# Performance work log

Hardware: AMD Instinct MI355X
Metric: run time of the kernel (lower is better)

## Reference

```python
import jax, jax.numpy as jnp
import numpy as np

B, T, N, M, P = 1024, 128, 128, 256, 256


def _lstm_step(x, h, c, Wih, Whh, bih, bhh):
    # PyTorch LSTM cell: gates ordered i, f, g, o
    g = x @ Wih.T + bih + h @ Whh.T + bhh
    i, f, gg, o = jnp.split(g, 4, axis=-1)
    c_new = jax.nn.sigmoid(f) * c + jax.nn.sigmoid(i) * jnp.tanh(gg)
    h_new = jax.nn.sigmoid(o) * jnp.tanh(c_new)
    return h_new, c_new


def darnn_forward(enc_data, dec_data, enc_Wih, enc_Whh, enc_bih, enc_bhh,
                  We, Ue, ve, Wd, Ud, vd, wt_w, wt_b,
                  dec_Wih, dec_Whh, dec_bih, dec_bhh, l1_w, l1_b, l2_w, l2_b):
    Bsz, Tlen, n = enc_data.shape
    m = enc_Whh.shape[1]
    p = dec_Whh.shape[1]
    # ---- Encoder with input attention ----
    # U_e(data.permute(0,2,1)): (B, n, T); constant across time steps
    Ue_data = jnp.einsum('btn,st->bns', enc_data, Ue)
    def enc_step(carry, x_t):
        h, c = carry                                   # (B, m) each
        q = jnp.concatenate([h, c], axis=-1)           # (B, 2m)
        wq = q @ We.T                                  # (B, T)
        score = jnp.tanh(wq[:, None, :] + Ue_data) @ ve  # (B, n)
        alpha = jax.nn.softmax(score, axis=-1)
        h, c = _lstm_step(alpha * x_t, h, c, enc_Wih, enc_Whh, enc_bih, enc_bhh)
        return (h, c), h
    h0 = jnp.zeros((Bsz, m), enc_data.dtype)
    (_, _), Hs = jax.lax.scan(enc_step, (h0, h0), jnp.swapaxes(enc_data, 0, 1))
    H = jnp.swapaxes(Hs, 0, 1)                         # (B, T, m)
    # ---- Decoder with temporal attention ----
    UH = jnp.einsum('btm,um->btu', H, Ud)              # (B, T, m); constant
    def attn_ctx(d, s):
        q = jnp.concatenate([d, s], axis=-1)           # (B, 2p)
        wq = q @ Wd.T                                  # (B, m)
        score = jnp.tanh(wq[:, None, :] + UH) @ vd     # (B, T)
        beta = jax.nn.softmax(score, axis=-1)
        return jnp.einsum('bt,btm->bm', beta, H)       # (B, m)
    def dec_step(carry, y):
        d, s = carry
        ctx = attn_ctx(d, s)
        y_tilde = jnp.concatenate([y, ctx], axis=-1) @ wt_w.T + wt_b  # (B, 1)
        d, s = _lstm_step(y_tilde, d, s, dec_Wih, dec_Whh, dec_bih, dec_bhh)
        return (d, s), None
    d0 = jnp.zeros((Bsz, p), enc_data.dtype)
    ys = jnp.swapaxes(dec_data[:, :Tlen - 1, :], 0, 1)  # (T-1, B, 1)
    (d, s), _ = jax.lax.scan(dec_step, (d0, d0), ys)
    ctx = attn_ctx(d, s)
    out = jnp.concatenate([d, ctx], axis=-1)            # (B, p + m)
    out = jax.nn.relu(out @ l1_w.T + l1_b) @ l2_w.T + l2_b
    return out.reshape(-1)


def setup_inputs() -> dict:
    key = jax.random.key(0)
    ks = jax.random.split(key, 22)
    f = lambda k, shape: jax.random.normal(k, shape, jnp.float32) * 0.05
    return {
        'enc_data': jax.random.normal(ks[0], (B, T, N), jnp.float32),
        'dec_data': jax.random.normal(ks[1], (B, T, 1), jnp.float32),
        'enc_Wih': f(ks[2], (4 * M, N)), 'enc_Whh': f(ks[3], (4 * M, M)),
        'enc_bih': f(ks[4], (4 * M,)), 'enc_bhh': f(ks[5], (4 * M,)),
        'We': f(ks[6], (T, 2 * M)), 'Ue': f(ks[7], (T, T)), 've': f(ks[8], (T,)),
        'Wd': f(ks[9], (M, 2 * P)), 'Ud': f(ks[10], (M, M)), 'vd': f(ks[11], (M,)),
        'wt_w': f(ks[12], (1, M + 1)), 'wt_b': f(ks[13], (1,)),
        'dec_Wih': f(ks[14], (4 * P, 1)), 'dec_Whh': f(ks[15], (4 * P, P)),
        'dec_bih': f(ks[16], (4 * P,)), 'dec_bhh': f(ks[17], (4 * P,)),
        'l1_w': f(ks[18], (P, M + P)), 'l1_b': f(ks[19], (P,)),
        'l2_w': f(ks[20], (1, P)), 'l2_b': f(ks[21], (1,)),
    }


def reference(enc_data, dec_data, enc_Wih, enc_Whh, enc_bih, enc_bhh,
              We, Ue, ve, Wd, Ud, vd, wt_w, wt_b,
              dec_Wih, dec_Whh, dec_bih, dec_bhh, l1_w, l1_b, l2_w, l2_b):
    return darnn_forward(enc_data, dec_data, enc_Wih, enc_Whh, enc_bih, enc_bhh,
                         We, Ue, ve, Wd, Ud, vd, wt_w, wt_b,
                         dec_Wih, dec_Whh, dec_bih, dec_bhh, l1_w, l1_b, l2_w, l2_b)
```

## Files before the change

kernel.cpp:

```cpp
#include <hip/hip_runtime.h>

typedef unsigned short ushort_t;
typedef unsigned char u8_t;
typedef unsigned int u32_t;
typedef float f32x2 __attribute__((ext_vector_type(2)));

static constexpr int BATCH = 1024;
static constexpr int TT = 128;
static constexpr int NN = 128;
static constexpr int MM = 256;

__device__ __forceinline__ float bf2f(ushort_t u) {
    union { unsigned int i; float f; } v;
    v.i = ((unsigned int)u) << 16;
    return v.f;
}
__device__ __forceinline__ ushort_t f2bf(float f) {
    union { unsigned int i; float f; } v;
    v.f = f;
    unsigned int i = v.i;
    return (ushort_t)((i + 0x7FFFu + ((i >> 16) & 1u)) >> 16);
}
__device__ __forceinline__ u32_t pk2bf(float lo, float hi) {
    return (u32_t)f2bf(lo) | ((u32_t)f2bf(hi) << 16);
}
__device__ __forceinline__ float dot2bf(u32_t a, u32_t b, float c) {
    float d;
    asm("v_dot2_f32_bf16 %0, %1, %2, %3" : "=v"(d) : "v"(a), "v"(b), "v"(c));
    return d;
}
__device__ __forceinline__ u32_t permb(u32_t s0, u32_t s1, u32_t sel) {
    u32_t d;
    asm("v_perm_b32 %0, %1, %2, %3" : "=v"(d) : "v"(s0), "v"(s1), "v"(sel));
    return d;
}
__device__ __forceinline__ void unp8(const int4 w, float* o) {
    union { unsigned int i; float f; } v;
    v.i = ((unsigned int)w.x) << 16;        o[0] = v.f;
    v.i = ((unsigned int)w.x) & 0xffff0000u; o[1] = v.f;
    v.i = ((unsigned int)w.y) << 16;        o[2] = v.f;
    v.i = ((unsigned int)w.y) & 0xffff0000u; o[3] = v.f;
    v.i = ((unsigned int)w.z) << 16;        o[4] = v.f;
    v.i = ((unsigned int)w.z) & 0xffff0000u; o[5] = v.f;
    v.i = ((unsigned int)w.w) << 16;        o[6] = v.f;
    v.i = ((unsigned int)w.w) & 0xffff0000u; o[7] = v.f;
}
__device__ __forceinline__ void unp4(const int2 w, float* o) {
    union { unsigned int i; float f; } v;
    v.i = ((unsigned int)w.x) << 16;        o[0] = v.f;
    v.i = ((unsigned int)w.x) & 0xffff0000u; o[1] = v.f;
    v.i = ((unsigned int)w.y) << 16;        o[2] = v.f;
    v.i = ((unsigned int)w.y) & 0xffff0000u; o[3] = v.f;
}
__device__ __forceinline__ void unp8f8(const int2 w, float* o) {
    f32x2 a = __builtin_amdgcn_cvt_pk_f32_fp8(w.x, false);
    f32x2 b = __builtin_amdgcn_cvt_pk_f32_fp8(w.x, true);
    f32x2 c = __builtin_amdgcn_cvt_pk_f32_fp8(w.y, false);
    f32x2 d = __builtin_amdgcn_cvt_pk_f32_fp8(w.y, true);
    o[0] = a.x; o[1] = a.y; o[2] = b.x; o[3] = b.y;
    o[4] = c.x; o[5] = c.y; o[6] = d.x; o[7] = d.y;
}
__device__ __forceinline__ float tanh_fast(float x) {
    float e = __expf(2.0f * x);
    return 1.0f - __fdividef(2.0f, e + 1.0f);
}
__device__ __forceinline__ float sig_fast(float x) {
    return __fdividef(1.0f, 1.0f + __expf(-x));
}

template<bool WBF16, bool TRANSW, int CMODE, bool RELU>
__global__ __launch_bounds__(256) void gemm_k(
    const float* __restrict__ A1, int lda1, long sA1z, int K1,
    const float* __restrict__ A2, int lda2, int K2,
    const void* __restrict__ W1v, int ldw1, long sW1z,
    const void* __restrict__ W2v, int ldw2,
    const float* __restrict__ bias1,
    void* __restrict__ Cv, int ldc, long sCz)
{
    __shared__ float As[32][68];
    __shared__ float Ws[32][68];
    const int tid = threadIdx.x;
    const int z = blockIdx.z;
    const int m0 = blockIdx.y * 64;
    const int g0 = blockIdx.x * 64;
    const int tm = tid & 15, tn = tid >> 4;
    float acc[4][4];
#pragma unroll
    for (int i = 0; i < 4; ++i)
#pragma unroll
        for (int j = 0; j < 4; ++j) acc[i][j] = 0.0f;

    for (int phase = 0; phase < 2; ++phase) {
        const float* A = (phase == 0) ? (A1 + (long)z * sA1z) : A2;
        const int lda = (phase == 0) ? lda1 : lda2;
        const int K = (phase == 0) ? K1 : K2;
        const int ldw = (phase == 0) ? ldw1 : ldw2;
        const void* Wv = (phase == 0) ? W1v : W2v;
        const long woff = (phase == 0) ? (long)z * sW1z : 0;
        if (A == nullptr || Wv == nullptr || K <= 0) continue;

        for (int k0 = 0; k0 < K; k0 += 32) {
            const int rem = K - k0;
            {
                const int tr0 = tid >> 3;
                const int tk = (tid & 7) * 4;
#pragma unroll
                for (int pass = 0; pass < 2; ++pass) {
                    const int m = tr0 + pass * 32;
                    const float* p = A + (long)(m0 + m) * lda + k0 + tk;
#pragma unroll
                    for (int j = 0; j < 4; ++j) {
                        float v = 0.0f;
                        if (tk + j < rem) v = p[j];
                        As[tk + j][m] = v;
                    }
                }
            }
            if constexpr (TRANSW) {
                const float* W = (const float*)Wv + woff;
                const int gq = (tid & 15) * 4;
                const int kr = tid >> 4;
#pragma unroll
                for (int pass = 0; pass < 2; ++pass) {
                    const int k = kr + pass * 16;
                    const float* p = W + (long)(k0 + k) * ldw + g0 + gq;
                    const bool ok = (k < rem);
#pragma unroll
                    for (int j = 0; j < 4; ++j) {
                        float v = 0.0f;
                        if (ok) v = p[j];
                        Ws[k][gq + j] = v;
                    }
                }
            } else if constexpr (WBF16) {
                const ushort_t* W = (const ushort_t*)Wv + woff;
                const int g = tid >> 2;
                const int tk = (tid & 3) * 8;
                const ushort_t* p = W + (long)(g0 + g) * ldw + k0 + tk;
#pragma unroll
                for (int j = 0; j < 8; ++j) {
                    float v = 0.0f;
                    if (tk + j < rem) v = bf2f(p[j]);
                    Ws[tk + j][g] = v;
                }
            } else {
                const float* W = (const float*)Wv + woff;
                const int tr0 = tid >> 3;
                const int tk = (tid & 7) * 4;
#pragma unroll
                for (int pass = 0; pass < 2; ++pass) {
                    const int g = tr0 + pass * 32;
                    const float* p = W + (long)(g0 + g) * ldw + k0 + tk;
#pragma unroll
                    for (int j = 0; j < 4; ++j) {
                        float v = 0.0f;
                        if (tk + j < rem) v = p[j];
                        Ws[tk + j][g] = v;
                    }
                }
            }
            __syncthreads();
#pragma unroll
            for (int kk = 0; kk < 32; ++kk) {
                const float4 av = *(const float4*)&As[kk][tm * 4];
                const float4 bv = *(const float4*)&Ws[kk][tn * 4];
                const float a[4] = {av.x, av.y, av.z, av.w};
                const float b[4] = {bv.x, bv.y, bv.z, bv.w};
#pragma unroll
                for (int i = 0; i < 4; ++i)
#pragma unroll
                    for (int j = 0; j < 4; ++j)
                        acc[i][j] = fmaf(a[i], b[j], acc[i][j]);
            }
            __syncthreads();
        }
    }
#pragma unroll
    for (int i = 0; i < 4; ++i) {
        const long m = m0 + tm * 4 + i;
        if constexpr (CMODE == 2) {
            float v[4];
#pragma unroll
            for (int j = 0; j < 4; ++j) {
                v[j] = acc[i][j];
                if (bias1) v[j] += bias1[g0 + tn * 4 + j];
                if (RELU) v[j] = fmaxf(v[j], 0.0f);
            }
            int pk = __builtin_amdgcn_cvt_pk_fp8_f32(v[0], v[1], 0, false);
            pk = __builtin_amdgcn_cvt_pk_fp8_f32(v[2], v[3], pk, true);
            *(unsigned int*)((u8_t*)Cv + (long)z * sCz + m * ldc + g0 + tn * 4) =
                (unsigned int)pk;
        } else {
#pragma unroll
            for (int j = 0; j < 4; ++j) {
                const int g = g0 + tn * 4 + j;
                float v = acc[i][j];
                if (bias1) v += bias1[g];
                if (RELU) v = fmaxf(v, 0.0f);
                if constexpr (CMODE == 1)
                    ((ushort_t*)Cv)[(long)z * sCz + m * ldc + g] = f2bf(v);
                else
                    ((float*)Cv)[(long)z * sCz + m * ldc + g] = v;
            }
        }
    }
}

__global__ void prep_encw_k(const float* __restrict__ Wih, const float* __restrict__ Whh,
                            ushort_t* __restrict__ dst) {
    int i = blockIdx.x * 256 + threadIdx.x;
    if (i >= 384 * 1024) return;
    int k = i >> 10, col = i & 1023, u = col >> 2, q = col & 3, g = q * 256 + u;
    float v = (k < 128) ? Wih[g * 128 + k] : Whh[g * 256 + (k - 128)];
    dst[(k >> 1) * 2048 + u * 8 + q * 2 + (k & 1)] = f2bf(v);
}

__global__ void prep_decw_k(const float* __restrict__ Wih, const float* __restrict__ Whh,
                            ushort_t* __restrict__ dst) {
    int i = blockIdx.x * 256 + threadIdx.x;
    if (i >= 257 * 1024) return;
    int k = i >> 10, col = i & 1023, u = col >> 2, q = col & 3, g = q * 256 + u;
    float v = (k == 0) ? Wih[g] : Whh[g * 256 + (k - 1)];
    ushort_t b = f2bf(v);
    if (k == 0) {
        dst[col] = b;
    } else {
        int kk = k - 1;
        dst[1024 + (kk >> 1) * 2048 + u * 8 + q * 2 + (kk & 1)] = b;
    }
}

__global__ void transpose_k(const float* __restrict__ src, float* __restrict__ dst,
                            int R, int C) {
    int i = blockIdx.x * 256 + threadIdx.x;
    if (i < R * C) { int r = i / C, c = i - r * C; dst[c * R + r] = src[i]; }
}

__global__ void packT_k(const float* __restrict__ src, ushort_t* __restrict__ dst,
                        int R, int C) {
    int i = blockIdx.x * 256 + threadIdx.x;
    if (i >= R * C) return;
    int s = i / C, k = i - s * C;
    dst[(k >> 1) * (2 * R) + (s >> 2) * 8 + (s & 3) * 2 + (k & 1)] = f2bf(src[i]);
}

__global__ __launch_bounds__(512) void enc_persist(
    const float* __restrict__ enc_data,
    const u8_t* __restrict__ D,
    const ushort_t* __restrict__ WeB,
    const float* __restrict__ ve,
    const ushort_t* __restrict__ WencB,
    const float* __restrict__ bih, const float* __restrict__ bhh,
    ushort_t* __restrict__ Hbf)
{
    const int tid = threadIdx.x;
    const int b0 = blockIdx.x * 4;
    __shared__ __align__(16) float cs[256][4];
    __shared__ __align__(16) u32_t qpk[256][4];
    __shared__ __align__(16) u32_t xtp[64][4];
    __shared__ __align__(16) float wqp[16][128][4];
    __shared__ __align__(16) float wqs[128][4];
    __shared__ __align__(16) float scp[8][4][128];
    __shared__ float gp[4][4][256];
    __shared__ float ves[128];

    if (tid < 128) ves[tid] = ve[tid];
    if (tid < 256) {
        const float4 z = make_float4(0.f, 0.f, 0.f, 0.f);
        *(float4*)cs[tid] = z;
    }
    {
        uint4 z4 = {0u, 0u, 0u, 0u};
        for (int i = tid; i < 256; i += 512) *(uint4*)qpk[i] = z4;
    }
    const int u = tid & 255;
    const int ks = tid >> 8;
    const float b_i = bih[u] + bhh[u];
    const float b_f = bih[256 + u] + bhh[256 + u];
    const float b_g = bih[512 + u] + bhh[512 + u];
    const float b_o = bih[768 + u] + bhh[768 + u];
    __syncthreads();

    const int kgq = tid >> 5, sv = tid & 31;
    const ushort_t* wq_w = WeB + (long)(kgq * 16) * 256 + sv * 8;
    const int nv = tid & 15, srow = (tid >> 4) & 3, ssl = tid >> 6;
    const u8_t* Dp0 = D + (long)(b0 + srow) * 16384 + (ssl * 16) * 128 + nv * 8;
    const ushort_t* gw = WencB + u * 8;

    float SVe = 0.0f;
#pragma unroll
    for (int s = 0; s < 16; ++s) SVe += ves[ssl * 16 + s];

    for (int t = 0; t < 128; ++t) {
        {
            float a[4][4];
#pragma unroll
            for (int m = 0; m < 4; ++m)
#pragma unroll
                for (int r = 0; r < 4; ++r) a[m][r] = 0.0f;
#pragma unroll 4
            for (int k2 = 0; k2 < 16; ++k2) {
                const uint4 wv = *(const uint4*)(wq_w + k2 * 256);
                const uint4 qv = *(const uint4*)qpk[kgq * 16 + k2];
                const u32_t wa[4] = {wv.x, wv.y, wv.z, wv.w};
                const u32_t qa[4] = {qv.x, qv.y, qv.z, qv.w};
#pragma unroll
                for (int m = 0; m < 4; ++m)
#pragma unroll
                    for (int r = 0; r < 4; ++r)
                        a[m][r] = dot2bf(wa[m], qa[r], a[m][r]);
            }
#pragma unroll
            for (int m = 0; m < 4; ++m)
                *(float4*)wqp[kgq][sv * 4 + m] = make_float4(a[m][0], a[m][1], a[m][2], a[m][3]);
        }
        __syncthreads();
        if (tid < 128) {
            float4 s = *(const float4*)wqp[0][tid];
#pragma unroll
            for (int g = 1; g < 16; ++g) {
                const float4 p = *(const float4*)wqp[g][tid];
                s.x += p.x; s.y += p.y; s.z += p.z; s.w += p.w;
            }
            *(float4*)wqs[tid] = s;
        }
        __syncthreads();
        {
            float a[8];
#pragma unroll
            for (int j = 0; j < 8; ++j) a[j] = 0.0f;
#pragma unroll 4
            for (int s = 0; s < 16; ++s) {
                const int sg = ssl * 16 + s;
                const float w2 = wqs[sg][srow] * 2.0f;
                const float vv = ves[sg];
                const int2 wv2 = *(const int2*)(Dp0 + s * 128);
                float d[8];
                unp8f8(wv2, d);
#pragma unroll
                for (int j = 0; j < 8; j += 2) {
                    const float eA = __expf(fminf(fmaf(d[j],     2.0f, w2), 43.0f));
                    const float eB = __expf(fminf(fmaf(d[j + 1], 2.0f, w2), 43.0f));
                    const float pA = eA + 1.0f, pB = eB + 1.0f;
                    const float rr = __fdividef(1.0f, pA * pB);
                    a[j]     = fmaf(vv, pB * rr, a[j]);
                    a[j + 1] = fmaf(vv, pA * rr, a[j + 1]);
                }
            }
            *(float4*)&scp[ssl][srow][nv * 8] =
                make_float4(fmaf(-2.f, a[0], SVe), fmaf(-2.f, a[1], SVe),
                            fmaf(-2.f, a[2], SVe), fmaf(-2.f, a[3], SVe));
            *(float4*)&scp[ssl][srow][nv * 8 + 4] =
                make_float4(fmaf(-2.f, a[4], SVe), fmaf(-2.f, a[5], SVe),
                            fmaf(-2.f, a[6], SVe), fmaf(-2.f, a[7], SVe));
        }
        __syncthreads();
        if (tid < 256) {
            const int w = tid >> 6, lane = tid & 63;
            float s0 = 0.0f, s1 = 0.0f;
#pragma unroll
            for (int g = 0; g < 8; ++g) {
                s0 += scp[g][w][lane];
                s1 += scp[g][w][lane + 64];
            }
            float mx = fmaxf(s0, s1);
            for (int o = 32; o > 0; o >>= 1) mx = fmaxf(mx, __shfl_xor(mx, o, 64));
            const float e0 = __expf(s0 - mx), e1 = __expf(s1 - mx);
            float sm = e0 + e1;
            for (int o = 32; o > 0; o >>= 1) sm += __shfl_xor(sm, o, 64);
            const float inv = __fdividef(1.0f, sm);
            const float* xp = enc_data + ((long)(b0 + w) * 128 + t) * 128;
            const float v0 = e0 * inv * xp[lane];
            const float v1 = e1 * inv * xp[lane + 64];
            const float p0 = __shfl_xor(v0, 1, 64);
            const float p1 = __shfl_xor(v1, 1, 64);
            if ((lane & 1) == 0) {
                xtp[lane >> 1][w] = pk2bf(v0, p0);
                xtp[32 + (lane >> 1)][w] = pk2bf(v1, p1);
            }
        }
        __syncthreads();
        float acc[4][4];
#pragma unroll
        for (int q = 0; q < 4; ++q)
#pragma unroll
            for (int r = 0; r < 4; ++r) acc[q][r] = 0.0f;
        if (ks == 0) {
#pragma unroll 4
            for (int p = 0; p < 64; ++p) {
                const uint4 wv = *(const uint4*)(gw + (long)p * 2048);
                const uint4 xv = *(const uint4*)xtp[p];
                const u32_t wa[4] = {wv.x, wv.y, wv.z, wv.w};
                const u32_t xa[4] = {xv.x, xv.y, xv.z, xv.w};
#pragma unroll
                for (int q = 0; q < 4; ++q)
#pragma unroll
                    for (int r = 0; r < 4; ++r)
                        acc[q][r] = dot2bf(wa[q], xa[r], acc[q][r]);
            }
#pragma unroll 4
            for (int p = 64; p < 96; ++p) {
                const uint4 wv = *(const uint4*)(gw + (long)p * 2048);
                const uint4 xv = *(const uint4*)qpk[p - 64];
                const u32_t wa[4] = {wv.x, wv.y, wv.z, wv.w};
                const u32_t xa[4] = {xv.x, xv.y, xv.z, xv.w};
#pragma unroll
                for (int q = 0; q < 4; ++q)
#pragma unroll
                    for (int r = 0; r < 4; ++r)
                        acc[q][r] = dot2bf(wa[q], xa[r], acc[q][r]);
            }
        } else {
#pragma unroll 4
            for (int p = 96; p < 192; ++p) {
                const uint4 wv = *(const uint4*)(gw + (long)p * 2048);
                const uint4 xv = *(const uint4*)qpk[p - 64];
                const u32_t wa[4] = {wv.x, wv.y, wv.z, wv.w};
                const u32_t xa[4] = {xv.x, xv.y, xv.z, xv.w};
#pragma unroll
                for (int q = 0; q < 4; ++q)
#pragma unroll
                    for (int r = 0; r < 4; ++r)
                        acc[q][r] = dot2bf(wa[q], xa[r], acc[q][r]);
            }
#pragma unroll
            for (int q = 0; q < 4; ++q)
#pragma unroll
                for (int r = 0; r < 4; ++r) gp[q][r][u] = acc[q][r];
        }
        __syncthreads();
        if (ks == 0) {
#pragma unroll
            for (int r = 0; r < 4; ++r) {
                const float iv = sig_fast(acc[0][r] + gp[0][r][u] + b_i);
                const float fv = sig_fast(acc[1][r] + gp[1][r][u] + b_f);
                const float gv = tanh_fast(acc[2][r] + gp[2][r][u] + b_g);
                const float ov = sig_fast(acc[3][r] + gp[3][r][u] + b_o);
                const float cn = fv * cs[u][r] + iv * gv;
                const float hn = ov * tanh_fast(cn);
                cs[u][r] = cn;
                const float hp = __shfl_xor(hn, 1, 64);
                const float cp = __shfl_xor(cn, 1, 64);
                if ((u & 1) == 0) {
                    qpk[u >> 1][r] = pk2bf(hn, hp);
                    qpk[128 + (u >> 1)][r] = pk2bf(cn, cp);
                }
                Hbf[((long)(b0 + r) * 128 + t) * 256 + u] = f2bf(hn);
            }
        }
        __syncthreads();
    }
}

__global__ __launch_bounds__(512) void dec_persist(
    const float* __restrict__ dec_data,
    const u8_t* __restrict__ UH2,
    const ushort_t* __restrict__ Hb,
    const ushort_t* __restrict__ WdB,
    const float* __restrict__ vd,
    const ushort_t* __restrict__ WdecB,
    const float* __restrict__ bih, const float* __restrict__ bhh,
    const float* __restrict__ wt_w, const float* __restrict__ wt_b,
    const float* __restrict__ l1T,
    const float* __restrict__ l1_b,
    const float* __restrict__ l2_w, const float* __restrict__ l2_b,
    float* __restrict__ out)
{
    const int tid = threadIdx.x;
    const int b0 = blockIdx.x * 4;
    __shared__ __align__(16) float ds4[256][4];
    __shared__ __align__(16) float ss4[256][4];
    __shared__ __align__(16) u32_t qpk[256][4];
    __shared__ __align__(16) float wqp[8][256][4];
    __shared__ __align__(16) float wqs[256][4];
    __shared__ __align__(16) float scp[8][4][128];
    __shared__ __align__(16) u32_t betap[64][4];
    __shared__ __align__(16) float ctxp[4][4][256];
    __shared__ __align__(16) float ctx4[256][4];
    __shared__ float gp[4][4][256];
    __shared__ __align__(16) float o14[256][4];
    __shared__ float vds[256];
    __shared__ float wt1s[256];
    __shared__ float l2s[256];
    __shared__ __align__(16) float yts[4];

    const int u = tid & 255;
    const int ks = tid >> 8;
    if (tid < 256) {
        vds[tid] = vd[tid];
        wt1s[tid] = wt_w[1 + tid];
        l2s[tid] = l2_w[tid];
        const float4 z = make_float4(0.f, 0.f, 0.f, 0.f);
        *(float4*)ds4[tid] = z;
        *(float4*)ss4[tid] = z;
    }
    {
        uint4 z4 = {0u, 0u, 0u, 0u};
        for (int i = tid; i < 256; i += 512) *(uint4*)qpk[i] = z4;
    }
    const float b_i = bih[u] + bhh[u];
    const float b_f = bih[256 + u] + bhh[256 + u];
    const float b_g = bih[512 + u] + bhh[512 + u];
    const float b_o = bih[768 + u] + bhh[768 + u];
    __syncthreads();

    const int kgq = tid >> 6, mv = tid & 63;
    const ushort_t* wq_w = WdB + (long)(kgq * 32) * 512 + mv * 8;
    const int tv = tid & 15, srow = (tid >> 4) & 3, usl = tid >> 6;
    const u8_t* up0 = UH2 + ((long)(b0 + srow) * 256 + usl * 32) * 128 + tv * 8;
    const int mv8 = tid & 31, crow = (tid >> 5) & 3, ssl2 = tid >> 7;
    const ushort_t* hp0 = Hb + ((long)(b0 + crow) * 128 + ssl2 * 32) * 256 + mv8 * 8;
    const ushort_t* gwp = WdecB + 1024 + u * 8;

    float SVd = 0.0f;
#pragma unroll
    for (int s = 0; s < 32; ++s) SVd += vds[usl * 32 + s];

    for (int td = 0; td < 128; ++td) {
        float gacc[4][4];
        {
            float a[4][4];
#pragma unroll
            for (int m = 0; m < 4; ++m)
#pragma unroll
                for (int r = 0; r < 4; ++r) a[m][r] = 0.0f;
#pragma unroll 4
            for (int k2 = 0; k2 < 32; ++k2) {
                const uint4 wv = *(const uint4*)(wq_w + k2 * 512);
                const uint4 qv = *(const uint4*)qpk[kgq * 32 + k2];
                const u32_t wa[4] = {wv.x, wv.y, wv.z, wv.w};
                const u32_t qa[4] = {qv.x, qv.y, qv.z, qv.w};
#pragma unroll
                for (int m = 0; m < 4; ++m)
#pragma unroll
                    for (int r = 0; r < 4; ++r)
                        a[m][r] = dot2bf(wa[m], qa[r], a[m][r]);
            }
#pragma unroll
            for (int m = 0; m < 4; ++m)
                *(float4*)wqp[kgq][mv * 4 + m] = make_float4(a[m][0], a[m][1], a[m][2], a[m][3]);
        }
        {
#pragma unroll
            for (int q = 0; q < 4; ++q)
#pragma unroll
                for (int r = 0; r < 4; ++r) gacc[q][r] = 0.0f;
            const int pbeg = ks * 64, pend = pbeg + 64;
#pragma unroll 4
            for (int p = pbeg; p < pend; ++p) {
                const uint4 wv = *(const uint4*)(gwp + (long)p * 2048);
                const uint4 xv = *(const uint4*)qpk[p];
                const u32_t wa[4] = {wv.x, wv.y, wv.z, wv.w};
                const u32_t xa[4] = {xv.x, xv.y, xv.z, xv.w};
#pragma unroll
                for (int q = 0; q < 4; ++q)
#pragma unroll
                    for (int r = 0; r < 4; ++r)
                        gacc[q][r] = dot2bf(wa[q], xa[r], gacc[q][r]);
            }
            if (ks != 0) {
#pragma unroll
                for (int q = 0; q < 4; ++q)
#pragma unroll
                    for (int r = 0; r < 4; ++r) gp[q][r][u] = gacc[q][r];
            }
        }
        __syncthreads();
        if (tid < 256) {
            float4 s = *(const float4*)wqp[0][tid];
#pragma unroll
            for (int g = 1; g < 8; ++g) {
                const float4 p = *(const float4*)wqp[g][tid];
                s.x += p.x; s.y += p.y; s.z += p.z; s.w += p.w;
            }
            *(float4*)wqs[tid] = s;
        }
        __syncthreads();
        {
            float a[8];
#pragma unroll
            for (int j = 0; j < 8; ++j) a[j] = 0.0f;
#pragma unroll 4
            for (int uu = 0; uu < 32; ++uu) {
                const int ug = usl * 32 + uu;
                const float w2 = wqs[ug][srow] * 2.0f;
                const float vv = vds[ug];
                const int2 wv2 = *(const int2*)(up0 + uu * 128);
                float d[8];
                unp8f8(wv2, d);
#pragma unroll
                for (int j = 0; j < 8; j += 2) {
                    const float eA = __expf(fminf(fmaf(d[j],     2.0f, w2), 43.0f));
                    const float eB = __expf(fminf(fmaf(d[j + 1], 2.0f, w2), 43.0f));
                    const float pA = eA + 1.0f, pB = eB + 1.0f;
                    const float rr = __fdividef(1.0f, pA * pB);
                    a[j]     = fmaf(vv, pB * rr, a[j]);
                    a[j + 1] = fmaf(vv, pA * rr, a[j + 1]);
                }
            }
            *(float4*)&scp[usl][srow][tv * 8] =
                make_float4(fmaf(-2.f, a[0], SVd), fmaf(-2.f, a[1], SVd),
                            fmaf(-2.f, a[2], SVd), fmaf(-2.f, a[3], SVd));
            *(float4*)&scp[usl][srow][tv * 8 + 4] =
                make_float4(fmaf(-2.f, a[4], SVd), fmaf(-2.f, a[5], SVd),
                            fmaf(-2.f, a[6], SVd), fmaf(-2.f, a[7], SVd));
        }
        __syncthreads();
        if (tid < 256) {
            const int w = tid >> 6, lane = tid & 63;
            float s0 = 0.0f, s1 = 0.0f;
#pragma unroll
            for (int g = 0; g < 8; ++g) {
                s0 += scp[g][w][lane];
                s1 += scp[g][w][lane + 64];
            }
            float mx = fmaxf(s0, s1);
            for (int o = 32; o > 0; o >>= 1) mx = fmaxf(mx, __shfl_xor(mx, o, 64));
            const float e0 = __expf(s0 - mx), e1 = __expf(s1 - mx);
            float sm = e0 + e1;
            for (int o = 32; o > 0; o >>= 1) sm += __shfl_xor(sm, o, 64);
            const float inv = __fdividef(1.0f, sm);
            const float bv0 = e0 * inv;
            const float bv1 = e1 * inv;
            const float q0 = __shfl_xor(bv0, 1, 64);
            const float q1 = __shfl_xor(bv1, 1, 64);
            if ((lane & 1) == 0) {
                betap[lane >> 1][w] = pk2bf(bv0, q0);
                betap[32 + (lane >> 1)][w] = pk2bf(bv1, q1);
            }
        }
        __syncthreads();
        {
            float c[8];
#pragma unroll
            for (int j = 0; j < 8; ++j) c[j] = 0.0f;
#pragma unroll 4
            for (int sp = 0; sp < 16; ++sp) {
                const u32_t bt = betap[ssl2 * 16 + sp][crow];
                const uint4 A = *(const uint4*)(hp0 + (2 * sp) * 256);
                const uint4 B = *(const uint4*)(hp0 + (2 * sp + 1) * 256);
                const u32_t Aa[4] = {A.x, A.y, A.z, A.w};
                const u32_t Ba[4] = {B.x, B.y, B.z, B.w};
#pragma unroll
                for (int x = 0; x < 4; ++x) {
                    const u32_t lo = permb(Aa[x], Ba[x], 0x01000504u);
                    const u32_t hi = permb(Aa[x], Ba[x], 0x03020706u);
                    c[2 * x]     = dot2bf(bt, lo, c[2 * x]);
                    c[2 * x + 1] = dot2bf(bt, hi, c[2 * x + 1]);
                }
            }
            *(float4*)&ctxp[ssl2][crow][mv8 * 8]     = make_float4(c[0], c[1], c[2], c[3]);
            *(float4*)&ctxp[ssl2][crow][mv8 * 8 + 4] = make_float4(c[4], c[5], c[6], c[7]);
        }
        __syncthreads();
        if (tid < 256) {
            const int m = tid;
            float cr[4];
#pragma unroll
            for (int r = 0; r < 4; ++r)
                cr[r] = ctxp[0][r][m] + ctxp[1][r][m] + ctxp[2][r][m] + ctxp[3][r][m];
            *(float4*)ctx4[m] = make_float4(cr[0], cr[1], cr[2], cr[3]);
        }
        __syncthreads();
        if (td == 127) break;
        if (tid < 256) {
            const int w = tid >> 6, lane = tid & 63;
            float s = ctx4[lane][w] * wt1s[lane]
                    + ctx4[lane + 64][w] * wt1s[lane + 64]
                    + ctx4[lane + 128][w] * wt1s[lane + 128]
                    + ctx4[lane + 192][w] * wt1s[lane + 192];
            for (int o = 32; o > 0; o >>= 1) s += __shfl_xor(s, o, 64);
            if (lane == 0)
                yts[w] = s + wt_b[0] + wt_w[0] * dec_data[(long)(b0 + w) * 128 + td];
        }
        __syncthreads();
        if (ks == 0) {
            float wy[4];
            unp4(*(const int2*)(WdecB + u * 4), wy);
            const float4 y4 = *(const float4*)yts;
            const float ya[4] = {y4.x, y4.y, y4.z, y4.w};
#pragma unroll
            for (int r = 0; r < 4; ++r) {
                const float iv = sig_fast(gacc[0][r] + gp[0][r][u] + wy[0] * ya[r] + b_i);
                const float fv = sig_fast(gacc[1][r] + gp[1][r][u] + wy[1] * ya[r] + b_f);
                const float gv = tanh_fast(gacc[2][r] + gp[2][r][u] + wy[2] * ya[r] + b_g);
                const float ov = sig_fast(gacc[3][r] + gp[3][r][u] + wy[3] * ya[r] + b_o);
                const float sn = fv * ss4[u][r] + iv * gv;
                const float dn = ov * tanh_fast(sn);
                ss4[u][r] = sn;
                ds4[u][r] = dn;
                const float dp = __shfl_xor(dn, 1, 64);
                const float sp = __shfl_xor(sn, 1, 64);
                if ((u & 1) == 0) {
                    qpk[u >> 1][r] = pk2bf(dn, dp);
                    qpk[128 + (u >> 1)][r] = pk2bf(sn, sp);
                }
            }
        }
        __syncthreads();
    }
    {
        const float* src = l1T + ks * 256 * 256;
        float a0 = 0, a1 = 0, a2 = 0, a3 = 0;
#pragma unroll 4
        for (int k = 0; k < 256; ++k) {
            const float w = src[k * 256 + u];
            const float4 q = (ks == 0) ? *(const float4*)ds4[k]
                                       : *(const float4*)ctx4[k];
            a0 = fmaf(q.x, w, a0); a1 = fmaf(q.y, w, a1);
            a2 = fmaf(q.z, w, a2); a3 = fmaf(q.w, w, a3);
        }
        if (ks == 1) {
            gp[0][0][u] = a0; gp[0][1][u] = a1; gp[0][2][u] = a2; gp[0][3][u] = a3;
        } else {
            gp[1][0][u] = a0; gp[1][1][u] = a1; gp[1][2][u] = a2; gp[1][3][u] = a3;
        }
    }
    __syncthreads();
    if (tid < 256) {
        const float bb = l1_b[tid];
        *(float4*)o14[tid] = make_float4(
            fmaxf(gp[0][0][tid] + gp[1][0][tid] + bb, 0.f),
            fmaxf(gp[0][1][tid] + gp[1][1][tid] + bb, 0.f),
            fmaxf(gp[0][2][tid] + gp[1][2][tid] + bb, 0.f),
            fmaxf(gp[0][3][tid] + gp[1][3][tid] + bb, 0.f));
    }
    __syncthreads();
    if (tid < 256) {
        const int w = tid >> 6, lane = tid & 63;
        float s = o14[lane][w] * l2s[lane]
                + o14[lane + 64][w] * l2s[lane + 64]
                + o14[lane + 128][w] * l2s[lane + 128]
                + o14[lane + 192][w] * l2s[lane + 192];
        for (int o = 32; o > 0; o >>= 1) s += __shfl_xor(s, o, 64);
        if (lane == 0) out[b0 + w] = s + l2_b[0];
    }
}

extern "C" void kernel_launch(void* const* d_in, const int* in_sizes, int n_in,
                              void* d_out, int out_size, void* d_ws, size_t ws_size,
                              hipStream_t stream)
{
    const float* enc_data = (const float*)d_in[0];
    const float* dec_data = (const float*)d_in[1];
    const float* enc_Wih  = (const float*)d_in[2];
    const float* enc_Whh  = (const float*)d_in[3];
    const float* enc_bih  = (const float*)d_in[4];
    const float* enc_bhh  = (const float*)d_in[5];
    const float* We   = (const float*)d_in[6];
    const float* Ue   = (const float*)d_in[7];
    const float* ve   = (const float*)d_in[8];
    const float* Wd   = (const float*)d_in[9];
    const float* Ud   = (const float*)d_in[10];
    const float* vd   = (const float*)d_in[11];
    const float* wt_w = (const float*)d_in[12];
    const float* wt_b = (const float*)d_in[13];
    const float* dec_Wih = (const float*)d_in[14];
    const float* dec_Whh = (const float*)d_in[15];
    const float* dec_bih = (const float*)d_in[16];
    const float* dec_bhh = (const float*)d_in[17];
    const float* l1_w = (const float*)d_in[18];
    const float* l1_b = (const float*)d_in[19];
    const float* l2_w = (const float*)d_in[20];
    const float* l2_b = (const float*)d_in[21];

    ushort_t* Hbf  = (ushort_t*)d_ws;
    u8_t* Dbf      = (u8_t*)(Hbf + (long)BATCH * TT * MM);
    u8_t* UHbf     = Dbf + (long)BATCH * TT * NN;
    ushort_t* WencB = (ushort_t*)(UHbf + (long)BATCH * MM * TT);
    ushort_t* WdecB = WencB + 384 * 1024;
    ushort_t* WeB   = WdecB + 257 * 1024;
    ushort_t* WdB   = WeB + 512 * 128;
    float* l1T      = (float*)(WdB + 512 * 256);

    prep_encw_k<<<1536, 256, 0, stream>>>(enc_Wih, enc_Whh, WencB);
    prep_decw_k<<<1028, 256, 0, stream>>>(dec_Wih, dec_Whh, WdecB);
    packT_k<<<(128 * 512 + 255) / 256, 256, 0, stream>>>(We, WeB, 128, 512);
    packT_k<<<(256 * 512 + 255) / 256, 256, 0, stream>>>(Wd, WdB, 256, 512);
    transpose_k<<<(256 * 512 + 255) / 256, 256, 0, stream>>>(l1_w, l1T, 256, 512);

    gemm_k<false, true, 2, false><<<dim3(NN / 64, TT / 64, BATCH), 256, 0, stream>>>(
        Ue, TT, 0, TT,
        nullptr, 0, 0,
        enc_data, NN, (long)TT * NN,
        nullptr, 0,
        nullptr,
        Dbf, NN, (long)TT * NN);

    enc_persist<<<256, 512, 0, stream>>>(enc_data, Dbf, WeB, ve, WencB,
                                         enc_bih, enc_bhh, Hbf);

    gemm_k<true, false, 2, false><<<dim3(TT / 64, MM / 64, BATCH), 256, 0, stream>>>(
        Ud, MM, 0, MM,
        nullptr, 0, 0,
        Hbf, MM, (long)TT * MM,
        nullptr, 0,
        nullptr,
        UHbf, TT, (long)MM * TT);

    dec_persist<<<256, 512, 0, stream>>>(dec_data, UHbf, Hbf, WdB, vd, WdecB,
                                         dec_bih, dec_bhh, wt_w, wt_b,
                                         l1T, l1_b, l2_w, l2_b, (float*)d_out);
}
```

Before: 8.004 ms.

## Prescale attention operands by 2·log2e and rebalance encoder gate GEMM across halves

Folds the 2·log2(e) factor of tanh into the packed We/Wd weights and the fp8 Ue·X and Ud·H projections, so the attention inner loop calls the raw v_exp_f32 on a plain add instead of a scaled __expf. In the encoder, the recurrent h/c part of the gate matvec is moved before the first barrier and split evenly across both thread halves, and the input part is also split in two. This overlaps work with the attention phase and balances the gate dot products, which were previously lopsided between ks halves. The fp8 storage now holds scaled values, which changes rounding and saturation range, and the clamp becomes 60.

```diff
diff --git a/kernel.cpp b/kernel.cpp
--- a/kernel.cpp
+++ b/kernel.cpp
@@ -9,6 +9,7 @@
 static constexpr int TT = 128;
 static constexpr int NN = 128;
 static constexpr int MM = 256;
+static constexpr float SC2LOG2E = 2.885390082f;
 
 __device__ __forceinline__ float bf2f(ushort_t u) {
     union { unsigned int i; float f; } v;
@@ -33,6 +34,11 @@
     u32_t d;
     asm("v_perm_b32 %0, %1, %2, %3" : "=v"(d) : "v"(s0), "v"(s1), "v"(sel));
     return d;
+}
+__device__ __forceinline__ float exp2_fast(float x) {
+    float r;
+    asm("v_exp_f32 %0, %1" : "=v"(r) : "v"(x));
+    return r;
 }
 __device__ __forceinline__ void unp8(const int4 w, float* o) {
     union { unsigned int i; float f; } v;
@@ -74,7 +80,7 @@
     const float* __restrict__ A2, int lda2, int K2,
     const void* __restrict__ W1v, int ldw1, long sW1z,
     const void* __restrict__ W2v, int ldw2,
-    const float* __restrict__ bias1,
+    const float* __restrict__ bias1, float oscale,
     void* __restrict__ Cv, int ldc, long sCz)
 {
     __shared__ float As[32][68];
@@ -182,7 +188,7 @@
             float v[4];
 #pragma unroll
             for (int j = 0; j < 4; ++j) {
-                v[j] = acc[i][j];
+                v[j] = acc[i][j] * oscale;
                 if (bias1) v[j] += bias1[g0 + tn * 4 + j];
                 if (RELU) v[j] = fmaxf(v[j], 0.0f);
             }
@@ -237,11 +243,11 @@
 }
 
 __global__ void packT_k(const float* __restrict__ src, ushort_t* __restrict__ dst,
-                        int R, int C) {
+                        int R, int C, float scale) {
     int i = blockIdx.x * 256 + threadIdx.x;
     if (i >= R * C) return;
     int s = i / C, k = i - s * C;
-    dst[(k >> 1) * (2 * R) + (s >> 2) * 8 + (s & 3) * 2 + (k & 1)] = f2bf(src[i]);
+    dst[(k >> 1) * (2 * R) + (s >> 2) * 8 + (s & 3) * 2 + (k & 1)] = f2bf(src[i] * scale);
 }
 
 __global__ __launch_bounds__(512) void enc_persist(
@@ -292,6 +298,11 @@
     for (int s = 0; s < 16; ++s) SVe += ves[ssl * 16 + s];
 
     for (int t = 0; t < 128; ++t) {
+        float gacc[4][4];
+#pragma unroll
+        for (int q = 0; q < 4; ++q)
+#pragma unroll
+            for (int r = 0; r < 4; ++r) gacc[q][r] = 0.0f;
         {
             float a[4][4];
 #pragma unroll
@@ -314,6 +325,21 @@
             for (int m = 0; m < 4; ++m)
                 *(float4*)wqp[kgq][sv * 4 + m] = make_float4(a[m][0], a[m][1], a[m][2], a[m][3]);
         }
+        {
+            const int pbeg = 64 + ks * 64, pend = pbeg + 64;
+#pragma unroll 4
+            for (int p = pbeg; p < pend; ++p) {
+                const uint4 wv = *(const uint4*)(gw + (long)p * 2048);
+                const uint4 xv = *(const uint4*)qpk[p - 64];
+                const u32_t wa[4] = {wv.x, wv.y, wv.z, wv.w};
+                const u32_t xa[4] = {xv.x, xv.y, xv.z, xv.w};
+#pragma unroll
+                for (int q = 0; q < 4; ++q)
+#pragma unroll
+                    for (int r = 0; r < 4; ++r)
+                        gacc[q][r] = dot2bf(wa[q], xa[r], gacc[q][r]);
+            }
+        }
         __syncthreads();
         if (tid < 128) {
             float4 s = *(const float4*)wqp[0][tid];
@@ -332,15 +358,15 @@
 #pragma unroll 4
             for (int s = 0; s < 16; ++s) {
                 const int sg = ssl * 16 + s;
-                const float w2 = wqs[sg][srow] * 2.0f;
+                const float w2 = wqs[sg][srow];
                 const float vv = ves[sg];
                 const int2 wv2 = *(const int2*)(Dp0 + s * 128);
                 float d[8];
                 unp8f8(wv2, d);
 #pragma unroll
                 for (int j = 0; j < 8; j += 2) {
-                    const float eA = __expf(fminf(fmaf(d[j],     2.0f, w2), 43.0f));
-                    const float eB = __expf(fminf(fmaf(d[j + 1], 2.0f, w2), 43.0f));
+                    const float eA = exp2_fast(fminf(d[j]     + w2, 60.0f));
+                    const float eB = exp2_fast(fminf(d[j + 1] + w2, 60.0f));
                     const float pA = eA + 1.0f, pB = eB + 1.0f;
                     const float rr = __fdividef(1.0f, pA * pB);
                     a[j]     = fmaf(vv, pB * rr, a[j]);
@@ -380,14 +406,10 @@
             }
         }
         __syncthreads();
-        float acc[4][4];
-#pragma unroll
-        for (int q = 0; q < 4; ++q)
-#pragma unroll
-            for (int r = 0; r < 4; ++r) acc[q][r] = 0.0f;
-        if (ks == 0) {
+        {
+            const int pbeg = ks * 32, pend = pbeg + 32;
 #pragma unroll 4
-            for (int p = 0; p < 64; ++p) {
+            for (int p = pbeg; p < pend; ++p) {
                 const uint4 wv = *(const uint4*)(gw + (long)p * 2048);
                 const uint4 xv = *(const uint4*)xtp[p];
                 const u32_t wa[4] = {wv.x, wv.y, wv.z, wv.w};
@@ -396,46 +418,23 @@
                 for (int q = 0; q < 4; ++q)
 #pragma unroll
                     for (int r = 0; r < 4; ++r)
-                        acc[q][r] = dot2bf(wa[q], xa[r], acc[q][r]);
-            }
-#pragma unroll 4
-            for (int p = 64; p < 96; ++p) {
-                const uint4 wv = *(const uint4*)(gw + (long)p * 2048);
-                const uint4 xv = *(const uint4*)qpk[p - 64];
-                const u32_t wa[4] = {wv.x, wv.y, wv.z, wv.w};
-                const u32_t xa[4] = {xv.x, xv.y, xv.z, xv.w};
+                        gacc[q][r] = dot2bf(wa[q], xa[r], gacc[q][r]);
+            }
+            if (ks != 0) {
 #pragma unroll
                 for (int q = 0; q < 4; ++q)
 #pragma unroll
-                    for (int r = 0; r < 4; ++r)
-                        acc[q][r] = dot2bf(wa[q], xa[r], acc[q][r]);
-            }
-        } else {
-#pragma unroll 4
-            for (int p = 96; p < 192; ++p) {
-                const uint4 wv = *(const uint4*)(gw + (long)p * 2048);
-                const uint4 xv = *(const uint4*)qpk[p - 64];
-                const u32_t wa[4] = {wv.x, wv.y, wv.z, wv.w};
-                const u32_t xa[4] = {xv.x, xv.y, xv.z, xv.w};
-#pragma unroll
-                for (int q = 0; q < 4; ++q)
-#pragma unroll
-                    for (int r = 0; r < 4; ++r)
-                        acc[q][r] = dot2bf(wa[q], xa[r], acc[q][r]);
-            }
-#pragma unroll
-            for (int q = 0; q < 4; ++q)
-#pragma unroll
-                for (int r = 0; r < 4; ++r) gp[q][r][u] = acc[q][r];
+                    for (int r = 0; r < 4; ++r) gp[q][r][u] = gacc[q][r];
+            }
         }
         __syncthreads();
         if (ks == 0) {
 #pragma unroll
             for (int r = 0; r < 4; ++r) {
-                const float iv = sig_fast(acc[0][r] + gp[0][r][u] + b_i);
-                const float fv = sig_fast(acc[1][r] + gp[1][r][u] + b_f);
-                const float gv = tanh_fast(acc[2][r] + gp[2][r][u] + b_g);
-                const float ov = sig_fast(acc[3][r] + gp[3][r][u] + b_o);
+                const float iv = sig_fast(gacc[0][r] + gp[0][r][u] + b_i);
+                const float fv = sig_fast(gacc[1][r] + gp[1][r][u] + b_f);
+                const float gv = tanh_fast(gacc[2][r] + gp[2][r][u] + b_g);
+                const float ov = sig_fast(gacc[3][r] + gp[3][r][u] + b_o);
                 const float cn = fv * cs[u][r] + iv * gv;
                 const float hn = ov * tanh_fast(cn);
                 cs[u][r] = cn;
@@ -583,15 +582,15 @@
 #pragma unroll 4
             for (int uu = 0; uu < 32; ++uu) {
                 const int ug = usl * 32 + uu;
-                const float w2 = wqs[ug][srow] * 2.0f;
+                const float w2 = wqs[ug][srow];
                 const float vv = vds[ug];
                 const int2 wv2 = *(const int2*)(up0 + uu * 128);
                 float d[8];
                 unp8f8(wv2, d);
 #pragma unroll
                 for (int j = 0; j < 8; j += 2) {
-                    const float eA = __expf(fminf(fmaf(d[j],     2.0f, w2), 43.0f));
-                    const float eB = __expf(fminf(fmaf(d[j + 1], 2.0f, w2), 43.0f));
+                    const float eA = exp2_fast(fminf(d[j]     + w2, 60.0f));
+                    const float eB = exp2_fast(fminf(d[j + 1] + w2, 60.0f));
                     const float pA = eA + 1.0f, pB = eB + 1.0f;
                     const float rr = __fdividef(1.0f, pA * pB);
                     a[j]     = fmaf(vv, pB * rr, a[j]);
@@ -775,8 +774,8 @@
 
     prep_encw_k<<<1536, 256, 0, stream>>>(enc_Wih, enc_Whh, WencB);
     prep_decw_k<<<1028, 256, 0, stream>>>(dec_Wih, dec_Whh, WdecB);
-    packT_k<<<(128 * 512 + 255) / 256, 256, 0, stream>>>(We, WeB, 128, 512);
-    packT_k<<<(256 * 512 + 255) / 256, 256, 0, stream>>>(Wd, WdB, 256, 512);
+    packT_k<<<(128 * 512 + 255) / 256, 256, 0, stream>>>(We, WeB, 128, 512, SC2LOG2E);
+    packT_k<<<(256 * 512 + 255) / 256, 256, 0, stream>>>(Wd, WdB, 256, 512, SC2LOG2E);
     transpose_k<<<(256 * 512 + 255) / 256, 256, 0, stream>>>(l1_w, l1T, 256, 512);
 
     gemm_k<false, true, 2, false><<<dim3(NN / 64, TT / 64, BATCH), 256, 0, stream>>>(
@@ -784,7 +783,7 @@
         nullptr, 0, 0,
         enc_data, NN, (long)TT * NN,
         nullptr, 0,
-        nullptr,
+        nullptr, SC2LOG2E,
         Dbf, NN, (long)TT * NN);
 
     enc_persist<<<256, 512, 0, stream>>>(enc_data, Dbf, WeB, ve, WencB,
@@ -795,7 +794,7 @@
         nullptr, 0, 0,
         Hbf, MM, (long)TT * MM,
         nullptr, 0,
-        nullptr,
+        nullptr, SC2LOG2E,
         UHbf, TT, (long)MM * TT);
 
     dec_persist<<<256, 512, 0, stream>>>(dec_data, UHbf, Hbf, WdB, vd, WdecB,
```

New measurement: 7.926 ms. About the same (-1.0%).
